# Kernel optimization log

Measured on AMD Instinct MI355X. Metric: run time of the kernel, lower is better.

## Reference

```python
import jax, jax.numpy as jnp
import numpy as np

DN = ('NCHW', 'OIHW', 'NCHW')

def dwconv(x, w, b, pad):
    # depthwise conv: w is [C,1,kh,kw], feature_group_count = C
    C = x.shape[1]
    y = jax.lax.conv_general_dilated(x, w, window_strides=(1, 1), padding=pad,
                                     dimension_numbers=DN, feature_group_count=C)
    return y + b[None, :, None, None]

KERNELS = [(5, 5), (1, 7), (7, 1), (1, 11), (11, 1), (1, 21), (21, 1)]

def setup_inputs() -> dict:
    key = jax.random.key(0)
    C = 384
    ks = jax.random.split(key, 20)
    inp = {'x': jax.random.normal(ks[0], (16, C, 64, 64), dtype=jnp.float32)}
    for i, (kh, kw) in enumerate(KERNELS):
        fan_in = kh * kw  # depthwise: in_channels/groups = 1
        bound = 1.0 / np.sqrt(fan_in)
        inp[f'w{i}'] = jax.random.uniform(ks[1 + 2 * i], (C, 1, kh, kw), minval=-bound, maxval=bound, dtype=jnp.float32)
        inp[f'b{i}'] = jax.random.uniform(ks[2 + 2 * i], (C,), minval=-bound, maxval=bound, dtype=jnp.float32)
    bound = 1.0 / np.sqrt(C)
    inp['wa'] = jax.random.uniform(ks[15], (C, C, 1, 1), minval=-bound, maxval=bound, dtype=jnp.float32)
    inp['ba'] = jax.random.uniform(ks[16], (C,), minval=-bound, maxval=bound, dtype=jnp.float32)
    return inp

def reference(x, w0, b0, w1, b1, w2, b2, w3, b3, w4, b4, w5, b5, w6, b6, wa, ba):
    # initial 5x5 depthwise
    initial = dwconv(x, w0, b0, ((2, 2), (2, 2)))
    pads = [((0, 0), (3, 3)), ((3, 3), (0, 0)), ((0, 0), (5, 5)),
            ((5, 5), (0, 0)), ((0, 0), (10, 10)), ((10, 10), (0, 0))]
    ws = [w1, w2, w3, w4, w5, w6]
    bs = [b1, b2, b3, b4, b5, b6]
    spatial = dwconv(initial, ws[0], bs[0], pads[0])
    for w, b, p in zip(ws[1:], bs[1:], pads[1:]):
        spatial = spatial + dwconv(initial, w, b, p)
    # 1x1 pointwise attention conv
    out = jax.lax.conv_general_dilated(spatial, wa, (1, 1), ((0, 0), (0, 0)), dimension_numbers=DN)
    return out + ba[None, :, None, None]
```

## Files before the change

kernel.cpp:

```cpp
#include <hip/hip_runtime.h>
#include <cstdint>

#define NBATCH 16
#define CCH    384
#define HW     64
#define PLANE  (HW*HW)
#define NTOT   (NBATCH*PLANE)
#define NPLANES (NBATCH*CCH)

typedef __attribute__((ext_vector_type(8))) short short8v;
typedef __attribute__((ext_vector_type(4))) float f32x4;

static __device__ __forceinline__ unsigned short f2bf(float f) {
    unsigned int x = __float_as_uint(f);
    unsigned int r = (x + 0x7fffu + ((x >> 16) & 1u)) >> 16;
    return (unsigned short)r;
}
static __device__ __forceinline__ unsigned int cvtpk(float a, float b) {
    unsigned int r;
    asm("v_cvt_pk_bf16_f32 %0, %1, %2" : "=v"(r) : "v"(a), "v"(b));
    return r;
}

static __device__ __forceinline__ int rotC(int row) {
    return 2 * (row >> 4) + (row & 7);
}

static __device__ __forceinline__ void conv5x5_lds8(const char* __restrict__ xs,
                                                    int h, int wb,
                                                    const float* __restrict__ w0c,
                                                    float bias, float out[8]) {
    #pragma unroll
    for (int q = 0; q < 8; ++q) out[q] = bias;
    #pragma unroll
    for (int i = 0; i < 5; ++i) {
        const int rt  = h + i - 2;
        const bool rok = (unsigned)rt < 64u;
        const int rm  = rt & 63;
        const int rx  = rm & 15;
        float f[16];
        #pragma unroll
        for (int g = 0; g < 4; ++g) {
            const int gq  = (wb >> 2) - 1 + g;
            const bool ok = rok && ((unsigned)gq < 16u);
            const int byte = rm * 256 + (((gq & 15) ^ rx) << 4);
            const float4 v = *reinterpret_cast<const float4*>(xs + byte);
            f[4*g+0] = ok ? v.x : 0.f;
            f[4*g+1] = ok ? v.y : 0.f;
            f[4*g+2] = ok ? v.z : 0.f;
            f[4*g+3] = ok ? v.w : 0.f;
        }
        #pragma unroll
        for (int j = 0; j < 5; ++j) {
            const float wg = w0c[i * 5 + j];
            #pragma unroll
            for (int q = 0; q < 8; ++q) out[q] += f[q + j + 2] * wg;
        }
    }
}

__global__ __launch_bounds__(256)
void prep(const float* __restrict__ w1, const float* __restrict__ b1,
          const float* __restrict__ w2, const float* __restrict__ b2,
          const float* __restrict__ w3, const float* __restrict__ b3,
          const float* __restrict__ w4, const float* __restrict__ b4,
          const float* __restrict__ w5, const float* __restrict__ b5,
          const float* __restrict__ w6, const float* __restrict__ b6,
          const float* __restrict__ wa, unsigned short* __restrict__ waB,
          unsigned short* __restrict__ fragV, unsigned short* __restrict__ fragH,
          float* __restrict__ bsum)
{
    const int tid = threadIdx.x;
    if (blockIdx.x >= CCH) {
        const int i = (blockIdx.x - CCH) * 256 + tid;
        const float4 v = reinterpret_cast<const float4*>(wa)[i];
        ushort4 o;
        o.x = f2bf(v.x); o.y = f2bf(v.y); o.z = f2bf(v.z); o.w = f2bf(v.w);
        reinterpret_cast<ushort4*>(waB)[i] = o;
        return;
    }
    const int c = blockIdx.x;
    __shared__ float swh[21];
    __shared__ float swv[21];

    if (tid < 21) {
        const int d = tid, dj = d - 10;
        float v = w5[c * 21 + d];
        if (dj >= -5 && dj <= 5) v += w3[c * 11 + dj + 5];
        if (dj >= -3 && dj <= 3) v += w1[c * 7  + dj + 3];
        swh[d] = v;
    } else if (tid >= 32 && tid < 53) {
        const int d = tid - 32, di = d - 10;
        float v = w6[c * 21 + d];
        if (di >= -5 && di <= 5) v += w4[c * 11 + di + 5];
        if (di >= -3 && di <= 3) v += w2[c * 7  + di + 3];
        swv[d] = v;
    } else if (tid == 64) {
        bsum[c] = b1[c] + b2[c] + b3[c] + b4[c] + b5[c] + b6[c];
    }
    __syncthreads();

    const int lane = tid & 63;
    const int slot = tid >> 6;
    const int l15  = lane & 15;
    const int l16  = lane >> 4;
    const int row  = slot * 16 + l15;

    #pragma unroll
    for (int kk = 0; kk < 2; ++kk) {
        unsigned short uv[8], uh[8];
        #pragma unroll
        for (int j = 0; j < 8; ++j) {
            const int k = kk * 32 + l16 * 8 + j;
            const int d = k - row + 10;
            const bool ok = (unsigned)d < 21u;
            uv[j] = ok ? f2bf(swv[d]) : (unsigned short)0;
            uh[j] = ok ? f2bf(swh[d]) : (unsigned short)0;
        }
        const size_t idx = (size_t)(((c * 4 + slot) * 2 + kk) * 64 + lane) * 8;
        *reinterpret_cast<uint4*>(fragV + idx) = *reinterpret_cast<const uint4*>(uv);
        *reinterpret_cast<uint4*>(fragH + idx) = *reinterpret_cast<const uint4*>(uh);
    }
}

__global__ __launch_bounds__(256)
void dw_fused(const float* __restrict__ x,
              const float* __restrict__ w0, const float* __restrict__ b0,
              const unsigned short* __restrict__ fragV,
              const unsigned short* __restrict__ fragH,
              const float* __restrict__ bsum,
              unsigned short* __restrict__ spB)
{
    __shared__ char sbuf[64 * 256];
    char* const xs  = sbuf;
    char* const ipR = sbuf;
    char* const ipT = sbuf + 8192;

    const int tid = threadIdx.x;
    const int n   = blockIdx.x / CCH;
    const int c   = blockIdx.x % CCH;

    const int lane = tid & 63;
    const int wid  = tid >> 6;
    const int l15  = lane & 15;
    const int l16  = lane >> 4;

    {
        const char* xb = (const char*)(x + (size_t)blockIdx.x * PLANE);
        const int sg = (((tid & 15) ^ (tid >> 4)) & 15) << 4;
        #pragma unroll
        for (int it = 0; it < 4; ++it) {
            const int row = it * 16 + (tid >> 4);
            const void* src = (const void*)(xb + row * 256 + sg);
            __builtin_amdgcn_global_load_lds(
                (const __attribute__((address_space(1))) void*)src,
                (__attribute__((address_space(3))) void*)(xs + it * 4096 + wid * 1024 + lane * 16),
                16, 0, 0);
        }
    }

    short8v aV[2];
    #pragma unroll
    for (int kk = 0; kk < 2; ++kk) {
        const size_t idx = (size_t)(((c * 4 + wid) * 2 + kk) * 64 + lane) * 8;
        aV[kk] = *reinterpret_cast<const short8v*>(fragV + idx);
    }

    const float b0v = b0[c];
    const float bv1 = bsum[c];
    const float* w0c = w0 + c * 25;

    __syncthreads();

    const int h  = tid >> 2;
    const int p  = tid & 3;
    const int ws = p << 4;

    unsigned int wv[8];
    {
        float accA[8];
        conv5x5_lds8(xs, h, ws, w0c, b0v, accA);
        #pragma unroll
        for (int j = 0; j < 4; ++j) wv[j] = cvtpk(accA[2*j], accA[2*j+1]);
    }
    {
        float accB[8];
        conv5x5_lds8(xs, h, ws + 8, w0c, b0v, accB);
        #pragma unroll
        for (int j = 0; j < 4; ++j) wv[4 + j] = cvtpk(accB[2*j], accB[2*j+1]);
    }
    __syncthreads();

    {
        const int rot = rotC(h);
        #pragma unroll
        for (int q = 0; q < 2; ++q) {
            const int off = ((ws << 1) + 16 * q + 16 * rot) & 127;
            uint4 u4 = make_uint4(wv[4*q+0], wv[4*q+1], wv[4*q+2], wv[4*q+3]);
            *reinterpret_cast<uint4*>(ipR + h * 128 + off) = u4;
        }
        #pragma unroll
        for (int k = 0; k < 16; ++k) {
            const int w   = ws + k;
            const int off = (2 * h + 16 * rotC(w)) & 127;
            *reinterpret_cast<unsigned short*>(ipT + w * 128 + off) =
                (unsigned short)(wv[k >> 1] >> (16 * (k & 1)));
        }
    }
    short8v bH[4][2];
    #pragma unroll
    for (int nt = 0; nt < 4; ++nt)
        #pragma unroll
        for (int kk = 0; kk < 2; ++kk) {
            const size_t idx = (size_t)(((c * 4 + nt) * 2 + kk) * 64 + lane) * 8;
            bH[nt][kk] = *reinterpret_cast<const short8v*>(fragH + idx);
        }
    __syncthreads();

    const int arow = wid * 16 + l15;
    const int rotA = 16 * (2 * wid + (l15 & 7));
    short8v aH[2];
    #pragma unroll
    for (int kk = 0; kk < 2; ++kk) {
        const int off = (kk * 64 + l16 * 16 + rotA) & 127;
        aH[kk] = *reinterpret_cast<const short8v*>(ipR + arow * 128 + off);
    }
    unsigned short* op = spB + ((size_t)c * NBATCH + n) * PLANE;

    #pragma unroll
    for (int nt = 0; nt < 4; ++nt) {
        const int brow = nt * 16 + l15;
        const int rotB = 16 * (2 * nt + (l15 & 7));
        f32x4 acc = (f32x4){0.f, 0.f, 0.f, 0.f};
        #pragma unroll
        for (int kk = 0; kk < 2; ++kk) {
            const int off = (kk * 64 + l16 * 16 + rotB) & 127;
            const short8v bV = *reinterpret_cast<const short8v*>(ipT + brow * 128 + off);
            acc = __builtin_amdgcn_mfma_f32_16x16x32_bf16(aV[kk], bV, acc, 0, 0, 0);
            acc = __builtin_amdgcn_mfma_f32_16x16x32_bf16(aH[kk], bH[nt][kk], acc, 0, 0, 0);
        }
        #pragma unroll
        for (int r = 0; r < 4; ++r) {
            const int hh = wid * 16 + 4 * l16 + r;
            const int ww = nt * 16 + l15;
            op[hh * HW + ww] = f2bf(acc[r] + bv1);
        }
    }
}

__global__ __launch_bounds__(256)
void pw_mfma(const unsigned short* __restrict__ spB,
             const unsigned short* __restrict__ waB,
             const float* __restrict__ ba, float* __restrict__ out)
{
    __shared__ unsigned short As[128 * 64];
    __shared__ unsigned short Bs[128 * 64];

    const int tid  = threadIdx.x;
    const int lane = tid & 63;
    const int wid  = tid >> 6;
    const int wrow = wid >> 1;
    const int wcol = wid & 1;

    const int co0  = blockIdx.y * 128;
    const int col0 = blockIdx.x * 128;

    f32x4 acc[4][4];
    #pragma unroll
    for (int m = 0; m < 4; ++m)
        #pragma unroll
        for (int nn = 0; nn < 4; ++nn) acc[m][nn] = (f32x4){0.f, 0.f, 0.f, 0.f};

    const char* waBb = (const char*)waB;

    for (int kt = 0; kt < 6; ++kt) {
        #pragma unroll
        for (int q = 0; q < 4; ++q) {
            const int L     = (wid * 4 + q) * 1024 + lane * 16;
            const int row   = L >> 7;
            const int kbyte = (L & 127) ^ ((row & 7) << 4);
            const void* src = (const void*)(waBb + (size_t)(co0 + row) * 768 + kt * 128 + kbyte);
            __builtin_amdgcn_global_load_lds(
                (const __attribute__((address_space(1))) void*)src,
                (__attribute__((address_space(3))) void*)((char*)As + (wid * 4 + q) * 1024),
                16, 0, 0);
        }

        #pragma unroll
        for (int j = 0; j < 2; ++j) {
            const int kloc  = j * 32 + 2 * (tid >> 4);
            const int cbase = 8 * (tid & 15);
            const unsigned int* gp =
                (const unsigned int*)(spB + (size_t)(kt * 64 + kloc) * NTOT + col0 + cbase);
            unsigned int g0[4], g1[4];
            *(uint4*)g0 = *(const uint4*)gp;
            *(uint4*)g1 = *(const uint4*)(gp + NTOT / 2);
            #pragma unroll
            for (int r = 0; r < 8; ++r) {
                const unsigned int w0v = g0[r >> 1], w1v = g1[r >> 1];
                const unsigned int lo = (r & 1) ? (w0v >> 16) : (w0v & 0xffffu);
                const unsigned int hi = (r & 1) ? (w1v >> 16) : (w1v & 0xffffu);
                const unsigned int val = lo | (hi << 16);
                const int colL = cbase + r;
                const int s    = (r ^ (tid & 7)) & 7;
                const int byte = colL * 128 + ((kloc * 2) ^ (s << 4));
                *(unsigned int*)((char*)Bs + byte) = val;
            }
        }
        __syncthreads();

        #pragma unroll
        for (int kk = 0; kk < 2; ++kk) {
            short8v aF[4], bF[4];
            const int kbyte = kk * 64 + (lane >> 4) * 16;
            #pragma unroll
            for (int m = 0; m < 4; ++m) {
                const int row = wrow * 64 + m * 16 + (lane & 15);
                aF[m] = *(const short8v*)((const char*)As + row * 128 + (kbyte ^ ((row & 7) << 4)));
            }
            #pragma unroll
            for (int nn = 0; nn < 4; ++nn) {
                const int col = wcol * 64 + nn * 16 + (lane & 15);
                const int s   = ((col & 7) ^ ((col >> 3) & 7)) << 4;
                bF[nn] = *(const short8v*)((const char*)Bs + col * 128 + (kbyte ^ s));
            }
            #pragma unroll
            for (int m = 0; m < 4; ++m)
                #pragma unroll
                for (int nn = 0; nn < 4; ++nn)
                    acc[m][nn] = __builtin_amdgcn_mfma_f32_16x16x32_bf16(
                        aF[m], bF[nn], acc[m][nn], 0, 0, 0);
        }
        __syncthreads();
    }

    const int nb  = col0 >> 12;
    const int px0 = col0 & 4095;
    #pragma unroll
    for (int m = 0; m < 4; ++m) {
        #pragma unroll
        for (int r = 0; r < 4; ++r) {
            const int co = co0 + wrow * 64 + m * 16 + 4 * (lane >> 4) + r;
            const float bv = ba[co];
            float* orow = out + ((size_t)(nb * CCH + co)) * PLANE + px0 + wcol * 64 + (lane & 15);
            #pragma unroll
            for (int nn = 0; nn < 4; ++nn)
                orow[nn * 16] = acc[m][nn][r] + bv;
        }
    }
}

extern "C" void kernel_launch(void* const* d_in, const int* in_sizes, int n_in,
                              void* d_out, int out_size, void* d_ws, size_t ws_size,
                              hipStream_t stream)
{
    const float* x  = (const float*)d_in[0];
    const float* w0 = (const float*)d_in[1];
    const float* b0 = (const float*)d_in[2];
    const float* w1 = (const float*)d_in[3];
    const float* b1 = (const float*)d_in[4];
    const float* w2 = (const float*)d_in[5];
    const float* b2 = (const float*)d_in[6];
    const float* w3 = (const float*)d_in[7];
    const float* b3 = (const float*)d_in[8];
    const float* w4 = (const float*)d_in[9];
    const float* b4 = (const float*)d_in[10];
    const float* w5 = (const float*)d_in[11];
    const float* b5 = (const float*)d_in[12];
    const float* w6 = (const float*)d_in[13];
    const float* b6 = (const float*)d_in[14];
    const float* wa = (const float*)d_in[15];
    const float* ba = (const float*)d_in[16];
    float* out = (float*)d_out;

    char* ws_base = (char*)d_ws;
    unsigned short* spB   = (unsigned short*)ws_base;
    unsigned short* waB   = (unsigned short*)(ws_base + 50331648);
    unsigned short* fragV = (unsigned short*)(ws_base + 50626560);
    unsigned short* fragH = (unsigned short*)(ws_base + 53772288);
    float*          bsum  = (float*)         (ws_base + 56918016);

    prep<<<dim3(CCH + 144), 256, 0, stream>>>(
        w1, b1, w2, b2, w3, b3, w4, b4, w5, b5, w6, b6, wa, waB, fragV, fragH, bsum);
    dw_fused<<<dim3(NPLANES), 256, 0, stream>>>(
        x, w0, b0, fragV, fragH, bsum, spB);
    pw_mfma<<<dim3(NTOT / 128, CCH / 128), 256, 0, stream>>>(spB, waB, ba, out);
}
```

Baseline: 95.09 us.

## Process two batch planes per block with prefetched second input plane

Each dw_fused block now handles two (n,c) planes of the same channel instead of one, halving the grid. The second plane's input is loaded asynchronously into a separate LDS buffer while the first plane is convolved and run through the MFMA stage. Per-channel weight fragments (fragV, fragH, bias) are loaded once and reused for both planes. LDS use per block rises from 16KB to 48KB, which may lower occupancy, and halving the block count reduces how much latency can be hidden across blocks.

```diff
diff --git a/kernel.cpp b/kernel.cpp
--- a/kernel.cpp
+++ b/kernel.cpp
@@ -6,7 +6,6 @@
 #define HW     64
 #define PLANE  (HW*HW)
 #define NTOT   (NBATCH*PLANE)
-#define NPLANES (NBATCH*CCH)
 
 typedef __attribute__((ext_vector_type(8))) short short8v;
 typedef __attribute__((ext_vector_type(4))) float f32x4;
@@ -131,32 +130,31 @@
               const float* __restrict__ bsum,
               unsigned short* __restrict__ spB)
 {
-    __shared__ char sbuf[64 * 256];
-    char* const xs  = sbuf;
-    char* const ipR = sbuf;
-    char* const ipT = sbuf + 8192;
+    __shared__ char xs0[64 * 256];
+    __shared__ char xs1[64 * 256];
+    __shared__ char ipR[64 * 128];
+    __shared__ char ipT[64 * 128];
 
     const int tid = threadIdx.x;
-    const int n   = blockIdx.x / CCH;
-    const int c   = blockIdx.x % CCH;
+    const int c   = blockIdx.x >> 3;
+    const int q   = blockIdx.x & 7;
 
     const int lane = tid & 63;
     const int wid  = tid >> 6;
     const int l15  = lane & 15;
     const int l16  = lane >> 4;
 
-    {
-        const char* xb = (const char*)(x + (size_t)blockIdx.x * PLANE);
-        const int sg = (((tid & 15) ^ (tid >> 4)) & 15) << 4;
-        #pragma unroll
-        for (int it = 0; it < 4; ++it) {
-            const int row = it * 16 + (tid >> 4);
-            const void* src = (const void*)(xb + row * 256 + sg);
-            __builtin_amdgcn_global_load_lds(
-                (const __attribute__((address_space(1))) void*)src,
-                (__attribute__((address_space(3))) void*)(xs + it * 4096 + wid * 1024 + lane * 16),
-                16, 0, 0);
-        }
+    const char* xb0 = (const char*)(x + ((size_t)q * CCH + c) * PLANE);
+    const char* xb1 = (const char*)(x + ((size_t)(q + 8) * CCH + c) * PLANE);
+    const int sg = (((tid & 15) ^ (tid >> 4)) & 15) << 4;
+
+    #pragma unroll
+    for (int it = 0; it < 4; ++it) {
+        const int row = it * 16 + (tid >> 4);
+        __builtin_amdgcn_global_load_lds(
+            (const __attribute__((address_space(1))) void*)(xb0 + row * 256 + sg),
+            (__attribute__((address_space(3))) void*)(xs0 + it * 4096 + wid * 1024 + lane * 16),
+            16, 0, 0);
     }
 
     short8v aV[2];
@@ -172,31 +170,42 @@
 
     __syncthreads();
 
+    #pragma unroll
+    for (int it = 0; it < 4; ++it) {
+        const int row = it * 16 + (tid >> 4);
+        __builtin_amdgcn_global_load_lds(
+            (const __attribute__((address_space(1))) void*)(xb1 + row * 256 + sg),
+            (__attribute__((address_space(3))) void*)(xs1 + it * 4096 + wid * 1024 + lane * 16),
+            16, 0, 0);
+    }
+
     const int h  = tid >> 2;
     const int p  = tid & 3;
     const int ws = p << 4;
+    const int rot = rotC(h);
+    const int arow = wid * 16 + l15;
+    const int rotA = 16 * (2 * wid + (l15 & 7));
+    unsigned short* const op0 = spB + ((size_t)c * NBATCH + q) * PLANE;
+    unsigned short* const op1 = spB + ((size_t)c * NBATCH + q + 8) * PLANE;
 
     unsigned int wv[8];
     {
         float accA[8];
-        conv5x5_lds8(xs, h, ws, w0c, b0v, accA);
+        conv5x5_lds8(xs0, h, ws, w0c, b0v, accA);
         #pragma unroll
         for (int j = 0; j < 4; ++j) wv[j] = cvtpk(accA[2*j], accA[2*j+1]);
     }
     {
         float accB[8];
-        conv5x5_lds8(xs, h, ws + 8, w0c, b0v, accB);
+        conv5x5_lds8(xs0, h, ws + 8, w0c, b0v, accB);
         #pragma unroll
         for (int j = 0; j < 4; ++j) wv[4 + j] = cvtpk(accB[2*j], accB[2*j+1]);
     }
-    __syncthreads();
-
-    {
-        const int rot = rotC(h);
-        #pragma unroll
-        for (int q = 0; q < 2; ++q) {
-            const int off = ((ws << 1) + 16 * q + 16 * rot) & 127;
-            uint4 u4 = make_uint4(wv[4*q+0], wv[4*q+1], wv[4*q+2], wv[4*q+3]);
+    {
+        #pragma unroll
+        for (int qq = 0; qq < 2; ++qq) {
+            const int off = ((ws << 1) + 16 * qq + 16 * rot) & 127;
+            uint4 u4 = make_uint4(wv[4*qq+0], wv[4*qq+1], wv[4*qq+2], wv[4*qq+3]);
             *reinterpret_cast<uint4*>(ipR + h * 128 + off) = u4;
         }
         #pragma unroll
@@ -217,33 +226,89 @@
         }
     __syncthreads();
 
-    const int arow = wid * 16 + l15;
-    const int rotA = 16 * (2 * wid + (l15 & 7));
-    short8v aH[2];
-    #pragma unroll
-    for (int kk = 0; kk < 2; ++kk) {
-        const int off = (kk * 64 + l16 * 16 + rotA) & 127;
-        aH[kk] = *reinterpret_cast<const short8v*>(ipR + arow * 128 + off);
-    }
-    unsigned short* op = spB + ((size_t)c * NBATCH + n) * PLANE;
-
-    #pragma unroll
-    for (int nt = 0; nt < 4; ++nt) {
-        const int brow = nt * 16 + l15;
-        const int rotB = 16 * (2 * nt + (l15 & 7));
-        f32x4 acc = (f32x4){0.f, 0.f, 0.f, 0.f};
+    {
+        short8v aH[2];
         #pragma unroll
         for (int kk = 0; kk < 2; ++kk) {
-            const int off = (kk * 64 + l16 * 16 + rotB) & 127;
-            const short8v bV = *reinterpret_cast<const short8v*>(ipT + brow * 128 + off);
-            acc = __builtin_amdgcn_mfma_f32_16x16x32_bf16(aV[kk], bV, acc, 0, 0, 0);
-            acc = __builtin_amdgcn_mfma_f32_16x16x32_bf16(aH[kk], bH[nt][kk], acc, 0, 0, 0);
-        }
-        #pragma unroll
-        for (int r = 0; r < 4; ++r) {
-            const int hh = wid * 16 + 4 * l16 + r;
-            const int ww = nt * 16 + l15;
-            op[hh * HW + ww] = f2bf(acc[r] + bv1);
+            const int off = (kk * 64 + l16 * 16 + rotA) & 127;
+            aH[kk] = *reinterpret_cast<const short8v*>(ipR + arow * 128 + off);
+        }
+        #pragma unroll
+        for (int nt = 0; nt < 4; ++nt) {
+            const int brow = nt * 16 + l15;
+            const int rotB = 16 * (2 * nt + (l15 & 7));
+            f32x4 acc = (f32x4){0.f, 0.f, 0.f, 0.f};
+            #pragma unroll
+            for (int kk = 0; kk < 2; ++kk) {
+                const int off = (kk * 64 + l16 * 16 + rotB) & 127;
+                const short8v bV = *reinterpret_cast<const short8v*>(ipT + brow * 128 + off);
+                acc = __builtin_amdgcn_mfma_f32_16x16x32_bf16(aV[kk], bV, acc, 0, 0, 0);
+                acc = __builtin_amdgcn_mfma_f32_16x16x32_bf16(aH[kk], bH[nt][kk], acc, 0, 0, 0);
+            }
+            #pragma unroll
+            for (int r = 0; r < 4; ++r) {
+                const int hh = wid * 16 + 4 * l16 + r;
+                const int ww = nt * 16 + l15;
+                op0[hh * HW + ww] = f2bf(acc[r] + bv1);
+            }
+        }
+    }
+    __syncthreads();
+
+    {
+        float accA[8];
+        conv5x5_lds8(xs1, h, ws, w0c, b0v, accA);
+        #pragma unroll
+        for (int j = 0; j < 4; ++j) wv[j] = cvtpk(accA[2*j], accA[2*j+1]);
+    }
+    {
+        float accB[8];
+        conv5x5_lds8(xs1, h, ws + 8, w0c, b0v, accB);
+        #pragma unroll
+        for (int j = 0; j < 4; ++j) wv[4 + j] = cvtpk(accB[2*j], accB[2*j+1]);
+    }
+    {
+        #pragma unroll
+        for (int qq = 0; qq < 2; ++qq) {
+            const int off = ((ws << 1) + 16 * qq + 16 * rot) & 127;
+            uint4 u4 = make_uint4(wv[4*qq+0], wv[4*qq+1], wv[4*qq+2], wv[4*qq+3]);
+            *reinterpret_cast<uint4*>(ipR + h * 128 + off) = u4;
+        }
+        #pragma unroll
+        for (int k = 0; k < 16; ++k) {
+            const int w   = ws + k;
+            const int off = (2 * h + 16 * rotC(w)) & 127;
+            *reinterpret_cast<unsigned short*>(ipT + w * 128 + off) =
+                (unsigned short)(wv[k >> 1] >> (16 * (k & 1)));
+        }
+    }
+    __syncthreads();
+
+    {
+        short8v aH[2];
+        #pragma unroll
+        for (int kk = 0; kk < 2; ++kk) {
+            const int off = (kk * 64 + l16 * 16 + rotA) & 127;
+            aH[kk] = *reinterpret_cast<const short8v*>(ipR + arow * 128 + off);
+        }
+        #pragma unroll
+        for (int nt = 0; nt < 4; ++nt) {
+            const int brow = nt * 16 + l15;
+            const int rotB = 16 * (2 * nt + (l15 & 7));
+            f32x4 acc = (f32x4){0.f, 0.f, 0.f, 0.f};
+            #pragma unroll
+            for (int kk = 0; kk < 2; ++kk) {
+                const int off = (kk * 64 + l16 * 16 + rotB) & 127;
+                const short8v bV = *reinterpret_cast<const short8v*>(ipT + brow * 128 + off);
+                acc = __builtin_amdgcn_mfma_f32_16x16x32_bf16(aV[kk], bV, acc, 0, 0, 0);
+                acc = __builtin_amdgcn_mfma_f32_16x16x32_bf16(aH[kk], bH[nt][kk], acc, 0, 0, 0);
+            }
+            #pragma unroll
+            for (int r = 0; r < 4; ++r) {
+                const int hh = wid * 16 + 4 * l16 + r;
+                const int ww = nt * 16 + l15;
+                op1[hh * HW + ww] = f2bf(acc[r] + bv1);
+            }
         }
     }
 }
@@ -382,7 +447,7 @@
 
     prep<<<dim3(CCH + 144), 256, 0, stream>>>(
         w1, b1, w2, b2, w3, b3, w4, b4, w5, b5, w6, b6, wa, waB, fragV, fragH, bsum);
-    dw_fused<<<dim3(NPLANES), 256, 0, stream>>>(
+    dw_fused<<<dim3(CCH * 8), 256, 0, stream>>>(
         x, w0, b0, fragV, fragH, bsum, spB);
     pw_mfma<<<dim3(NTOT / 128, CCH / 128), 256, 0, stream>>>(spB, waB, ba, out);
 }
```

After: 97.36 us. 2.4% more time.
